# Kernel tuning notes

Measured on AMD Instinct MI355X. Metric: run time of the kernel, lower is better.

## Reference

```python
import jax, jax.numpy as jnp
import numpy as np

B, T, C, H, HD = 2, 2048, 1024, 16, 64
EPS = 1e-6

def rmsnorm(x):
    return x * jax.lax.rsqrt(jnp.mean(x * x, axis=-1, keepdims=True) + EPS)

def rotary_cos_sin(seq_len, hd):
    inv_freq = 1.0 / (10000.0 ** (jnp.arange(0, hd, 2, dtype=jnp.float32) / hd))
    freqs = jnp.arange(seq_len, dtype=jnp.float32)[:, None] * inv_freq[None, :]  # [T, hd/2]
    return jnp.cos(freqs)[None, :, None, :], jnp.sin(freqs)[None, :, None, :]

def apply_rotary(x, cos, sin):
    x1, x2 = x[..., : HD // 2], x[..., HD // 2 :]
    return jnp.concatenate([x1 * cos + x2 * sin, -x1 * sin + x2 * cos], axis=-1)


def setup_inputs() -> dict:
    key = jax.random.key(0)
    ks = jax.random.split(key, 8)
    return {
        "x": jax.random.normal(ks[0], (B, T, C), jnp.float32),
        "w_qkv": jax.random.normal(ks[1], (3 * C, C), jnp.float32) * 0.02,
        "w_out": jax.random.normal(ks[2], (C, C), jnp.float32) * 0.02,
        "hyp_curvature": jax.random.uniform(ks[3], (1, H, 1, 1), jnp.float32, 0.5, 1.5),
        "w_uv": jax.random.normal(ks[4], (8 * C, C), jnp.float32) * 0.02,
        "b_uv": jnp.zeros((8 * C,), jnp.float32),
        "w_mlp_out": jax.random.normal(ks[5], (C, 4 * C), jnp.float32) * 0.02,
        "b_mlp_out": jnp.zeros((C,), jnp.float32),
    }


def reference(x, w_qkv, w_out, hyp_curvature, w_uv, b_uv, w_mlp_out, b_mlp_out):
    # --- pre-norm (euc/hyp branch uses rms_norm) ---
    h = rmsnorm(x)
    # --- QKV projection ---
    qkv = h @ w_qkv.T  # [B,T,3C]
    q, k, v = jnp.split(qkv, 3, axis=-1)
    q = q.reshape(B, T, H, HD)
    k = k.reshape(B, T, H, HD)
    v = v.reshape(B, T, H, HD)
    # --- RoPE ---
    cos, sin = rotary_cos_sin(T, HD)
    q = apply_rotary(q, cos, sin)
    k = apply_rotary(k, cos, sin)
    # [B,H,T,HD]
    q = jnp.transpose(q, (0, 2, 1, 3))
    k = jnp.transpose(k, (0, 2, 1, 3))
    v = jnp.transpose(v, (0, 2, 1, 3))
    # --- hyperbolic (Lorentz) attention ---
    kc = hyp_curvature  # [1,H,1,1], positive per-head curvature
    q0 = jnp.sqrt(kc + jnp.sum(q * q, axis=-1, keepdims=True))  # time coord [B,H,T,1]
    k0 = jnp.sqrt(kc + jnp.sum(k * k, axis=-1, keepdims=True))
    # Lorentz inner product <u,v>_L = -u0*v0 + u.v  -> [B,H,T,S]
    lorentz = jnp.einsum("bhtd,bhsd->bhts", q, k) - q0 * jnp.swapaxes(k0, -1, -2)
    dis = jnp.sqrt(kc) * jnp.arccosh(jnp.maximum(-lorentz / kc, 1.0 + EPS))
    causal = jnp.tril(jnp.ones((T, T), dtype=bool))
    scores = jnp.where(causal, -dis, -jnp.inf)  # hyp_attn_weight='neg_dis'
    attn_w = jax.nn.softmax(scores, axis=-1)
    attn = jnp.einsum("bhts,bhsd->bhtd", attn_w, v)
    attn = jnp.transpose(attn, (0, 2, 1, 3)).reshape(B, T, C)
    x = x + attn @ w_out.T
    # --- SwiGLU MLP with pre rms_norm ---
    h = rmsnorm(x)
    uv = h @ w_uv.T + b_uv
    u, vg = jnp.split(uv, 2, axis=-1)
    h_mlp = (u * jax.nn.silu(vg)) @ w_mlp_out.T + b_mlp_out
    return x + h_mlp
```

## Files before the change

### kernel.cpp

```cpp
#include <hip/hip_runtime.h>
#include <cstdint>
#include <cmath>

typedef __bf16 bf16;
typedef __attribute__((ext_vector_type(8))) __bf16 bf16x8;
typedef __attribute__((ext_vector_type(4))) __bf16 bf16x4;
typedef __attribute__((ext_vector_type(2))) __bf16 bf16x2;
typedef __attribute__((ext_vector_type(4))) float f32x4;

constexpr int B_ = 2, T_ = 2048, C_ = 1024, H_ = 16, HD_ = 64;
constexpr int M_ = B_ * T_;

#define EXP2F(x) __builtin_amdgcn_exp2f(x)
#define LOG2F(x) __builtin_amdgcn_logf(x)
#define SQRTF(x) __builtin_amdgcn_sqrtf(x)
#define RCPF(x)  __builtin_amdgcn_rcpf(x)

__device__ __forceinline__ void gld16(const void* g, void* l) {
  __builtin_amdgcn_global_load_lds((const __attribute__((address_space(1))) void*)g,
                                   (__attribute__((address_space(3))) void*)l, 16, 0, 0);
}

__global__ __launch_bounds__(256) void cast_all_kernel(const float* __restrict__ s0,
                                                       const float* __restrict__ s1,
                                                       const float* __restrict__ s2,
                                                       const float* __restrict__ s3,
                                                       const float* __restrict__ s4,
                                                       bf16* __restrict__ d0,
                                                       bf16* __restrict__ d1,
                                                       bf16* __restrict__ d2,
                                                       bf16* __restrict__ d3,
                                                       float* __restrict__ d4) {
  size_t gid = (size_t)blockIdx.x * 256 + threadIdx.x;
  if (gid >= 786432 + 262144 + 2097152 + 1048576) {
    size_t g4 = gid - (786432 + 262144 + 2097152 + 1048576);
    if (g4 >= 2048) return;
    int r = (int)(g4 * 4);
    int dr;
    if (r < 4096) { int g = r >> 5, i = r & 31; dr = g * 64 + i; }
    else { int j = r - 4096; int g = j >> 5, i = j & 31; dr = g * 64 + 32 + i; }
    *(f32x4*)(d4 + dr) = *(const f32x4*)(s4 + r);
    return;
  }
  const float* src;
  bf16* dst;
  size_t dstoff;
  if (gid < 786432) { src = s0; dst = d0; dstoff = gid * 4; }
  else if (gid < 786432 + 262144) { gid -= 786432; src = s1; dst = d1; dstoff = gid * 4; }
  else if (gid < 786432 + 262144 + 2097152) {
    gid -= 786432 + 262144; src = s2; dst = d2;
    size_t elem = gid * 4;
    int r = (int)(elem >> 10), c = (int)(elem & 1023);
    int dr;
    if (r < 4096) { int g = r >> 5, i = r & 31; dr = g * 64 + i; }
    else { int j = r - 4096; int g = j >> 5, i = j & 31; dr = g * 64 + 32 + i; }
    dstoff = ((size_t)dr << 10) | (size_t)c;
  }
  else { gid -= 786432 + 262144 + 2097152; src = s3; dst = d3; dstoff = gid * 4; }
  f32x4 v = *(const f32x4*)(src + gid * 4);
  bf16x4 o;
  o[0] = (bf16)v[0]; o[1] = (bf16)v[1]; o[2] = (bf16)v[2]; o[3] = (bf16)v[3];
  *(bf16x4*)(dst + dstoff) = o;
}

template <int MODE, typename OutT, int BM = 128>
__global__ __launch_bounds__(256) void gemm_bt(const bf16* __restrict__ A,
                                               const bf16* __restrict__ Bw,
                                               OutT* __restrict__ Cmat,
                                               const float* __restrict__ bias,
                                               const float* __restrict__ R,
                                               int M, int N, int K, int lda) {
  __shared__ __align__(16) bf16 shmem[(2 * BM + 2 * 128) * 32];
  bf16* const AlsH[2] = { &shmem[0], &shmem[BM * 32] };
  bf16* const BlsH[2] = { &shmem[2 * BM * 32], &shmem[2 * BM * 32 + 4096] };
  const int tid  = threadIdx.x;
  const int wave = tid >> 6;
  const int lane = tid & 63;
  const int quad = lane >> 4;
  const int l16  = lane & 15;
  const int bm = blockIdx.x * BM;
  const int bn = blockIdx.y * 128;
  const int wm = (wave & 1) * (BM / 2);
  const int wn = (wave >> 1) * 64;
  const int srow   = lane >> 2;
  const int schunk = lane & 3;
  constexpr int MT = BM / 32;

  f32x4 acc[MT][4];
#pragma unroll
  for (int i = 0; i < MT; i++)
#pragma unroll
    for (int j = 0; j < 4; j++) acc[i][j] = f32x4{0.f, 0.f, 0.f, 0.f};

  const bf16* Ag = A  + (size_t)(bm + wave * (BM / 4) + srow) * lda + schunk * 8;
  const bf16* Bg = Bw + (size_t)(bn + wave * 32 + srow) * K   + schunk * 8;
  bf16* AlsW0 = AlsH[0] + (wave * (BM / 4)) * 32;
  bf16* AlsW1 = AlsH[1] + (wave * (BM / 4)) * 32;
  bf16* BlsW0 = BlsH[0] + (wave * 32) * 32;
  bf16* BlsW1 = BlsH[1] + (wave * 32) * 32;

  for (int k0 = 0; k0 < K; k0 += 64) {
    gld16(Ag + k0, AlsW0);
    if (BM == 128) gld16(Ag + k0 + (size_t)16 * lda, AlsW0 + 16 * 32);
    gld16(Ag + k0 + 32, AlsW1);
    if (BM == 128) gld16(Ag + k0 + 32 + (size_t)16 * lda, AlsW1 + 16 * 32);
    gld16(Bg + k0,                       BlsW0);
    gld16(Bg + k0 + (size_t)16 * K,      BlsW0 + 16 * 32);
    gld16(Bg + k0 + 32,                  BlsW1);
    gld16(Bg + k0 + 32 + (size_t)16 * K, BlsW1 + 16 * 32);
    __syncthreads();

#pragma unroll
    for (int hh = 0; hh < 2; hh++) {
      bf16x8 af[MT], bfr[4];
#pragma unroll
      for (int mt = 0; mt < MT; mt++)
        af[mt] = *(const bf16x8*)&AlsH[hh][(wm + mt * 16 + l16) * 32 + quad * 8];
#pragma unroll
      for (int nt = 0; nt < 4; nt++)
        bfr[nt] = *(const bf16x8*)&BlsH[hh][(wn + nt * 16 + l16) * 32 + quad * 8];
#pragma unroll
      for (int mt = 0; mt < MT; mt++)
#pragma unroll
        for (int nt = 0; nt < 4; nt++)
          acc[mt][nt] = __builtin_amdgcn_mfma_f32_16x16x32_bf16(af[mt], bfr[nt], acc[mt][nt], 0, 0, 0);
    }
    __syncthreads();
  }

#pragma unroll
  for (int mt = 0; mt < MT; mt++) {
    const int row = bm + wm + mt * 16 + quad * 4;
#pragma unroll
    for (int nt = 0; nt < 4; nt++) {
      const int col = bn + wn + nt * 16 + l16;
      float bval = 0.f;
      if (MODE & 2) bval = bias[col];
#pragma unroll
      for (int r = 0; r < 4; r++) {
        float v = acc[mt][nt][r] + bval;
        if (MODE & 1) v += R[(size_t)(row + r) * N + col];
        Cmat[(size_t)(row + r) * N + col] = (OutT)v;
      }
    }
  }
}

__global__ __launch_bounds__(512, 2) void gemm8_swiglu(const bf16* __restrict__ A,
                                                       const bf16* __restrict__ Bw,
                                                       bf16* __restrict__ Cmat,
                                                       const float* __restrict__ bias) {
  constexpr int K = 1024, NTILE = K / 64;
  __shared__ __align__(16) bf16 smem[2][2][256][64];

  const int tid  = threadIdx.x;
  const int wave = tid >> 6, lane = tid & 63;
  const int quad = lane >> 4, l16 = lane & 15;
  const int wm = wave >> 2, wn = wave & 3;
  const int bm = blockIdx.x * 256;
  const int bn = blockIdx.y * 256;

  const int csw = (tid & 7) ^ ((tid >> 3) & 7);
  const bf16* gA = A  + (size_t)(bm + (tid >> 3)) * K + csw * 8;
  const bf16* gB = Bw + (size_t)(bn + (tid >> 3)) * K + csw * 8;
  const int wrow = wave * 8;

  const int r7 = l16 & 7;

  f32x4 acc[8][4];
#pragma unroll
  for (int i = 0; i < 8; i++)
#pragma unroll
    for (int j = 0; j < 4; j++) acc[i][j] = f32x4{0.f, 0.f, 0.f, 0.f};

#define STAGE8(buf_, tile_, h_) do {                                          \
    const int mat_ = (h_) >> 1;                                               \
    const int r0_  = ((h_) & 1) * 128;                                        \
    const bf16* s_ = (mat_ ? gB : gA) + (size_t)r0_ * K + (size_t)(tile_) * 64; \
    bf16* d_ = &smem[buf_][mat_][r0_ + wrow][0];                              \
    gld16(s_, d_);                                                            \
    gld16(s_ + (size_t)64 * K, d_ + 64 * 64);                                 \
  } while (0)

  STAGE8(0, 0, 0); STAGE8(0, 0, 1); STAGE8(0, 0, 2); STAGE8(0, 0, 3);
  STAGE8(1, 1, 0);
  asm volatile("s_waitcnt vmcnt(2)" ::: "memory");
  asm volatile("s_barrier" ::: "memory");

  bf16x8 af[4], bfr[4];
#pragma unroll 1
  for (int t = 0; t < NTILE; ++t) {
    const int buf = t & 1;
#pragma unroll
    for (int ph = 0; ph < 4; ph++) {
      const int ks = ph >> 1, mh = ph & 1;
      if (mh == 0) {
#pragma unroll
        for (int nt = 0; nt < 4; nt++)
          bfr[nt] = *(const bf16x8*)
              &smem[buf][1][wn * 64 + nt * 16 + l16][((ks * 4 + nt * 0 + quad) ^ r7) * 8];
      }
#pragma unroll
      for (int i = 0; i < 4; i++)
        af[i] = *(const bf16x8*)
            &smem[buf][0][wm * 128 + (mh * 4 + i) * 16 + l16][((ks * 4 + quad) ^ r7) * 8];
      if (ph < 3 && t + 1 < NTILE) STAGE8(buf ^ 1, t + 1, ph + 1);
      asm volatile("s_barrier" ::: "memory");
      asm volatile("s_waitcnt lgkmcnt(0)" ::: "memory");
      __builtin_amdgcn_sched_barrier(0);
      __builtin_amdgcn_s_setprio(1);
#pragma unroll
      for (int i = 0; i < 4; i++)
#pragma unroll
        for (int nt = 0; nt < 4; nt++)
          acc[mh * 4 + i][nt] =
              __builtin_amdgcn_mfma_f32_16x16x32_bf16(af[i], bfr[nt], acc[mh * 4 + i][nt], 0, 0, 0);
      __builtin_amdgcn_s_setprio(0);
      __builtin_amdgcn_sched_barrier(0);
      asm volatile("s_barrier" ::: "memory");
    }
    if (t + 1 < NTILE) {
      if (t + 2 < NTILE) {
        STAGE8(buf, t + 2, 0);
        asm volatile("s_waitcnt vmcnt(2)" ::: "memory");
      } else {
        asm volatile("s_waitcnt vmcnt(0)" ::: "memory");
      }
      asm volatile("s_barrier" ::: "memory");
    }
  }
#undef STAGE8

  const int cg = (bn >> 1) + wn * 32;
#pragma unroll
  for (int ntl = 0; ntl < 2; ntl++) {
    const float bu = bias[bn + wn * 64 + ntl * 16 + l16];
    const float bv = bias[bn + wn * 64 + 32 + ntl * 16 + l16];
    const int col = cg + ntl * 16 + l16;
#pragma unroll
    for (int mt = 0; mt < 8; mt++) {
      const int row = bm + wm * 128 + mt * 16 + quad * 4;
#pragma unroll
      for (int r = 0; r < 4; r++) {
        float u = acc[mt][ntl][r] + bu;
        float v = acc[mt][ntl + 2][r] + bv;
        float sig = RCPF(1.f + EXP2F(-v * 1.44269504f));
        Cmat[(size_t)(row + r) * 4096 + col] = (bf16)(u * v * sig);
      }
    }
  }
}

__global__ __launch_bounds__(256) void rmsnorm_kernel(const float* __restrict__ X,
                                                      bf16* __restrict__ O) {
  const int row = blockIdx.x;
  const int tid = threadIdx.x;
  const int wave = tid >> 6;
  f32x4 v = *(const f32x4*)(X + (size_t)row * C_ + tid * 4);
  float s = v[0] * v[0] + v[1] * v[1] + v[2] * v[2] + v[3] * v[3];
#pragma unroll
  for (int off = 32; off >= 1; off >>= 1) s += __shfl_xor(s, off);
  __shared__ float wsum[4];
  __shared__ float scale_sh;
  if ((tid & 63) == 0) wsum[wave] = s;
  __syncthreads();
  if (tid == 0)
    scale_sh = rsqrtf((wsum[0] + wsum[1] + wsum[2] + wsum[3]) * (1.f / (float)C_) + 1e-6f);
  __syncthreads();
  const float sc = scale_sh;
  bf16x4 o;
  o[0] = (bf16)(v[0] * sc); o[1] = (bf16)(v[1] * sc);
  o[2] = (bf16)(v[2] * sc); o[3] = (bf16)(v[3] * sc);
  *(bf16x4*)(O + (size_t)row * C_ + tid * 4) = o;
}

__global__ __launch_bounds__(256) void rotary_kernel(bf16* __restrict__ qkv,
                                                     const float* __restrict__ kcb,
                                                     float* __restrict__ q0b,
                                                     float* __restrict__ k0b) {
  const int wid  = blockIdx.x * 4 + (threadIdx.x >> 6);
  const int lane = threadIdx.x & 63;
  const int b = wid >> 15;
  const int rem = wid & 32767;
  const int t = rem >> 4;
  const int h = rem & 15;
  const int i = lane & 31;
  const float invf = expf(-((float)i / 32.f) * 9.210340371976184f);
  const float ang = (float)t * invf;
  const float cx = cosf(ang), sx = sinf(ang);
  const float kc = kcb[h];
  bf16* qp = qkv + (size_t)(b * T_ + t) * 3072 + h * 64;

#pragma unroll
  for (int which = 0; which < 2; which++) {
    bf16* p = qp + which * 1024;
    float x1 = (float)p[i];
    float x2 = (float)p[i + 32];
    float o = (lane < 32) ? (x1 * cx + x2 * sx) : (x2 * cx - x1 * sx);
    float ss = o * o;
#pragma unroll
    for (int off = 32; off >= 1; off >>= 1) ss += __shfl_xor(ss, off);
    p[lane] = (bf16)o;
    if (lane == 0) {
      float* dst = which == 0 ? q0b : k0b;
      dst[(size_t)(b * H_ + h) * T_ + t] = SQRTF(kc + ss);
    }
  }
}

__global__ __launch_bounds__(512) void attn_kernel(const bf16* __restrict__ qkv,
                                                   const float* __restrict__ q0b,
                                                   const float* __restrict__ k0b,
                                                   const float* __restrict__ kcb,
                                                   bf16* __restrict__ outp) {
  __shared__ __align__(16) bf16 Kls[2][64][72];
  __shared__ __align__(16) bf16 Vt[2][64][68];
  __shared__ __align__(16) bf16 Pls[8][16 * 36];
  __shared__ float k0s[2][64];

  const int tid = threadIdx.x;
  const int wave = tid >> 6, lane = tid & 63;
  const int quad = lane >> 4, l16 = lane & 15;
  const int bh = blockIdx.x;
  const int b = bh >> 4, h = bh & 15;

  const float kc = kcb[h];
  const float inv_kc = 1.f / kc;
  const float sqkc = SQRTF(kc);
  const int role = tid >> 8;
  const int st = tid & 255;
  const int sp = st & 31, dq = st >> 5;
  bf16* Pl = Pls[wave];
  const float* q0base = q0b + (size_t)(b * H_ + h) * T_;
  const float* k0base = k0b + (size_t)(b * H_ + h) * T_;

  const int ty = 15 - (int)blockIdx.y;
  const int t0 = ty * 128;
  const int tb = t0 + wave * 16;
  const int nIter = 2 * ty + 2;

  const bf16* qrow = qkv + (size_t)(b * T_ + tb + l16) * 3072 + h * 64;
  bf16x8 aq0 = *(const bf16x8*)(qrow + quad * 8);
  bf16x8 aq1 = *(const bf16x8*)(qrow + 32 + quad * 8);
  float q0r[4];
#pragma unroll
  for (int r = 0; r < 4; r++) q0r[r] = q0base[tb + quad * 4 + r];

  f32x4 o[4];
#pragma unroll
  for (int dt = 0; dt < 4; dt++) o[dt] = f32x4{0.f, 0.f, 0.f, 0.f};
  float lrow[4] = {0.f, 0.f, 0.f, 0.f};

  const bf16* base = qkv + (size_t)b * T_ * 3072 + 1024 + role * 1024 + h * 64 + dq * 8;
  bf16x8 pf_a = *(const bf16x8*)(base + (size_t)(2 * sp) * 3072);
  bf16x8 pf_b = *(const bf16x8*)(base + (size_t)(2 * sp + 1) * 3072);
  float k0v = (tid < 64) ? k0base[tid] : 0.f;

  for (int it = 0; it < nIter; ++it) {
    const int s0 = it * 64;
    const int buf = it & 1;
    if (role == 0) {
      *(bf16x8*)&Kls[buf][2 * sp][dq * 8]     = pf_a;
      *(bf16x8*)&Kls[buf][2 * sp + 1][dq * 8] = pf_b;
    } else {
#pragma unroll
      for (int i2 = 0; i2 < 8; i2++) {
        bf16x2 pr;
        pr[0] = pf_a[i2];
        pr[1] = pf_b[i2];
        *(bf16x2*)&Vt[buf][dq * 8 + i2][2 * sp] = pr;
      }
    }
    if (tid < 64) k0s[buf][tid] = k0v;
    __syncthreads();

    const int s0n = (it + 1 < nIter) ? s0 + 64 : s0;
    pf_a = *(const bf16x8*)(base + (size_t)(s0n + 2 * sp) * 3072);
    pf_b = *(const bf16x8*)(base + (size_t)(s0n + 2 * sp + 1) * 3072);
    if (tid < 64) k0v = k0base[s0n + tid];

    if (s0 <= tb + 15) {
      f32x4 sc[4];
#pragma unroll
      for (int nt = 0; nt < 4; nt++) {
        sc[nt] = f32x4{0.f, 0.f, 0.f, 0.f};
        bf16x8 b0 = *(const bf16x8*)&Kls[buf][nt * 16 + l16][quad * 8];
        bf16x8 b1 = *(const bf16x8*)&Kls[buf][nt * 16 + l16][32 + quad * 8];
        sc[nt] = __builtin_amdgcn_mfma_f32_16x16x32_bf16(aq0, b0, sc[nt], 0, 0, 0);
        sc[nt] = __builtin_amdgcn_mfma_f32_16x16x32_bf16(aq1, b1, sc[nt], 0, 0, 0);
      }

      bf16x8 ap[2];
#pragma unroll
      for (int ck = 0; ck < 2; ck++) {
#pragma unroll
        for (int ntl = 0; ntl < 2; ntl++) {
          const int nt = ck * 2 + ntl;
          const float k0c = k0s[buf][nt * 16 + l16];
          const int s = s0 + nt * 16 + l16;
#pragma unroll
          for (int r = 0; r < 4; r++) {
            const int t = tb + quad * 4 + r;
            float lor = sc[nt][r] - q0r[r] * k0c;
            float ratio = fmaxf(-lor * inv_kc, 1.f + 1e-6f);
            float wv = ratio + SQRTF(ratio * ratio - 1.f);
            float p = EXP2F(-sqkc * LOG2F(wv));
            p = (s <= t) ? p : 0.f;
            lrow[r] += p;
            Pl[(quad * 4 + r) * 36 + ntl * 16 + l16] = (bf16)p;
          }
        }
        ap[ck] = *(const bf16x8*)&Pl[l16 * 36 + quad * 8];
      }
#pragma unroll
      for (int dt = 0; dt < 4; dt++) {
        bf16x8 bv0 = *(const bf16x8*)&Vt[buf][dt * 16 + l16][quad * 8];
        bf16x8 bv1 = *(const bf16x8*)&Vt[buf][dt * 16 + l16][32 + quad * 8];
        o[dt] = __builtin_amdgcn_mfma_f32_16x16x32_bf16(ap[0], bv0, o[dt], 0, 0, 0);
        o[dt] = __builtin_amdgcn_mfma_f32_16x16x32_bf16(ap[1], bv1, o[dt], 0, 0, 0);
      }
    }
  }

#pragma unroll
  for (int r = 0; r < 4; r++) {
#pragma unroll
    for (int off = 1; off <= 8; off <<= 1) lrow[r] += __shfl_xor(lrow[r], off);
  }
#pragma unroll
  for (int r = 0; r < 4; r++) {
    const float invl = RCPF(lrow[r]);
    const int t = tb + quad * 4 + r;
#pragma unroll
    for (int dt = 0; dt < 4; dt++) {
      float val = o[dt][r] * invl;
      outp[(size_t)(b * T_ + t) * C_ + h * 64 + dt * 16 + l16] = (bf16)val;
    }
  }
}

extern "C" void kernel_launch(void* const* d_in, const int* in_sizes, int n_in,
                              void* d_out, int out_size, void* d_ws, size_t ws_size,
                              hipStream_t stream) {
  const float* x      = (const float*)d_in[0];
  const float* w_qkv  = (const float*)d_in[1];
  const float* w_out  = (const float*)d_in[2];
  const float* kcb    = (const float*)d_in[3];
  const float* w_uv   = (const float*)d_in[4];
  const float* b_uv   = (const float*)d_in[5];
  const float* w_mlp  = (const float*)d_in[6];
  const float* b_mlp  = (const float*)d_in[7];
  float* out = (float*)d_out;

  const size_t MB = 1024ull * 1024ull;
  char* w = (char*)d_ws;
  bf16*  wqkv_b  = (bf16*)(w + 0);
  bf16*  wout_b  = (bf16*)(w + 6 * MB);
  bf16*  wuv_p   = (bf16*)(w + 8 * MB);
  bf16*  wmlp_b  = (bf16*)(w + 24 * MB);
  bf16*  hbuf    = (bf16*)(w + 32 * MB);
  bf16*  qkvbuf  = (bf16*)(w + 40 * MB);
  bf16*  attnbuf = (bf16*)(w + 64 * MB);
  bf16*  gbuf    = (bf16*)(w + 40 * MB);
  float* x2buf   = (float*)(w + 72 * MB);
  float* q0b     = (float*)(w + 88 * MB);
  float* k0b     = (float*)(w + 88 * MB + 256 * 1024);
  float* biasp   = (float*)(w + 88 * MB + 512 * 1024);

  const int total4 = 786432 + 262144 + 2097152 + 1048576 + 2048;
  cast_all_kernel<<<(total4 + 255) / 256, 256, 0, stream>>>(
      w_qkv, w_out, w_uv, w_mlp, b_uv, wqkv_b, wout_b, wuv_p, wmlp_b, biasp);

  rmsnorm_kernel<<<M_, 256, 0, stream>>>(x, hbuf);
  gemm_bt<0, bf16><<<dim3(M_ / 128, 3072 / 128), 256, 0, stream>>>(
      hbuf, wqkv_b, qkvbuf, nullptr, nullptr, M_, 3072, 1024, 1024);
  rotary_kernel<<<(B_ * T_ * H_) / 4, 256, 0, stream>>>(qkvbuf, kcb, q0b, k0b);
  attn_kernel<<<dim3(B_ * H_, 16), 512, 0, stream>>>(qkvbuf, q0b, k0b, kcb, attnbuf);
  gemm_bt<1, float, 64><<<dim3(M_ / 64, 1024 / 128), 256, 0, stream>>>(
      attnbuf, wout_b, x2buf, nullptr, x, M_, 1024, 1024, 1024);
  rmsnorm_kernel<<<M_, 256, 0, stream>>>(x2buf, hbuf);
  gemm8_swiglu<<<dim3(M_ / 256, 8192 / 256), 512, 0, stream>>>(hbuf, wuv_p, gbuf, biasp);
  gemm_bt<3, float, 64><<<dim3(M_ / 64, 1024 / 128), 256, 0, stream>>>(
      gbuf, wmlp_b, out, b_mlp, x2buf, M_, 1024, 4096, 4096);
}
```

Baseline: 405.4 us.

## Restructure SwiGLU GEMM pipeline: full-tile prefetch, register double-buffered fragments, fewer barriers

The up-projection GEMM mainloop now issues all global-to-LDS loads for tile t+2 in one batch after finishing tile t, instead of interleaving a quarter of the staging into each of the four compute phases. The per-phase barriers, lgkmcnt waits and sched_barriers are removed. LDS fragments are read into double-buffered register arrays so the reads for later phases overlap the current MFMAs. This cuts synchronisation overhead and lets the compiler schedule LDS reads under MFMA work, at the cost of higher register pressure and less smooth spreading of global traffic across the loop.

```diff
diff --git a/kernel.cpp b/kernel.cpp
--- a/kernel.cpp
+++ b/kernel.cpp
@@ -181,54 +181,68 @@
     gld16(s_, d_);                                                            \
     gld16(s_ + (size_t)64 * K, d_ + 64 * 64);                                 \
   } while (0)
-
-  STAGE8(0, 0, 0); STAGE8(0, 0, 1); STAGE8(0, 0, 2); STAGE8(0, 0, 3);
-  STAGE8(1, 1, 0);
-  asm volatile("s_waitcnt vmcnt(2)" ::: "memory");
+#define STAGE_ALL(buf_, tile_) do {                                           \
+    STAGE8(buf_, tile_, 0); STAGE8(buf_, tile_, 1);                           \
+    STAGE8(buf_, tile_, 2); STAGE8(buf_, tile_, 3); } while (0)
+
+  STAGE_ALL(0, 0);
+  STAGE_ALL(1, 1);
+  asm volatile("s_waitcnt vmcnt(8)" ::: "memory");
   asm volatile("s_barrier" ::: "memory");
 
-  bf16x8 af[4], bfr[4];
 #pragma unroll 1
   for (int t = 0; t < NTILE; ++t) {
     const int buf = t & 1;
+    bf16x8 afX[2][4], bfX[2][4];
+#pragma unroll
+    for (int nt = 0; nt < 4; nt++)
+      bfX[0][nt] = *(const bf16x8*)&smem[buf][1][wn * 64 + nt * 16 + l16][(quad ^ r7) * 8];
+#pragma unroll
+    for (int i = 0; i < 4; i++)
+      afX[0][i] = *(const bf16x8*)&smem[buf][0][wm * 128 + i * 16 + l16][(quad ^ r7) * 8];
+
 #pragma unroll
     for (int ph = 0; ph < 4; ph++) {
-      const int ks = ph >> 1, mh = ph & 1;
-      if (mh == 0) {
+      const int mh = ph & 1;
+      const int ks = ph >> 1;
+      if (ph == 0) {
+#pragma unroll
+        for (int i = 0; i < 4; i++)
+          afX[1][i] = *(const bf16x8*)&smem[buf][0][wm * 128 + (4 + i) * 16 + l16][(quad ^ r7) * 8];
+      } else if (ph == 1) {
 #pragma unroll
         for (int nt = 0; nt < 4; nt++)
-          bfr[nt] = *(const bf16x8*)
-              &smem[buf][1][wn * 64 + nt * 16 + l16][((ks * 4 + nt * 0 + quad) ^ r7) * 8];
-      }
-#pragma unroll
-      for (int i = 0; i < 4; i++)
-        af[i] = *(const bf16x8*)
-            &smem[buf][0][wm * 128 + (mh * 4 + i) * 16 + l16][((ks * 4 + quad) ^ r7) * 8];
-      if (ph < 3 && t + 1 < NTILE) STAGE8(buf ^ 1, t + 1, ph + 1);
-      asm volatile("s_barrier" ::: "memory");
-      asm volatile("s_waitcnt lgkmcnt(0)" ::: "memory");
-      __builtin_amdgcn_sched_barrier(0);
+          bfX[1][nt] = *(const bf16x8*)&smem[buf][1][wn * 64 + nt * 16 + l16][((4 + quad) ^ r7) * 8];
+#pragma unroll
+        for (int i = 0; i < 4; i++)
+          afX[0][i] = *(const bf16x8*)&smem[buf][0][wm * 128 + i * 16 + l16][((4 + quad) ^ r7) * 8];
+      } else if (ph == 2) {
+#pragma unroll
+        for (int i = 0; i < 4; i++)
+          afX[1][i] = *(const bf16x8*)&smem[buf][0][wm * 128 + (4 + i) * 16 + l16][((4 + quad) ^ r7) * 8];
+      }
       __builtin_amdgcn_s_setprio(1);
 #pragma unroll
       for (int i = 0; i < 4; i++)
 #pragma unroll
         for (int nt = 0; nt < 4; nt++)
           acc[mh * 4 + i][nt] =
-              __builtin_amdgcn_mfma_f32_16x16x32_bf16(af[i], bfr[nt], acc[mh * 4 + i][nt], 0, 0, 0);
+              __builtin_amdgcn_mfma_f32_16x16x32_bf16(afX[mh][i], bfX[ks][nt], acc[mh * 4 + i][nt], 0, 0, 0);
       __builtin_amdgcn_s_setprio(0);
-      __builtin_amdgcn_sched_barrier(0);
+    }
+
+    if (t + 1 < NTILE) {
       asm volatile("s_barrier" ::: "memory");
-    }
-    if (t + 1 < NTILE) {
       if (t + 2 < NTILE) {
-        STAGE8(buf, t + 2, 0);
-        asm volatile("s_waitcnt vmcnt(2)" ::: "memory");
+        STAGE_ALL(buf, t + 2);
+        asm volatile("s_waitcnt vmcnt(8)" ::: "memory");
       } else {
         asm volatile("s_waitcnt vmcnt(0)" ::: "memory");
       }
       asm volatile("s_barrier" ::: "memory");
     }
   }
+#undef STAGE_ALL
 #undef STAGE8
 
   const int cg = (bn >> 1) + wn * 32;
```

Measured after the change: 396.0 us. -2.3%, faster.
